# Kernel optimization log

Hardware: AMD Instinct MI355X
Metric: run time of the kernel (lower is better)

Reference implementation:

```python
import jax, jax.numpy as jnp
import numpy as np

HEADS = 8
DIM_K = 64
DIM_G = 64
INPLANES = 512
PLANES = 128  # int(inplanes * ratio)


def setup_inputs() -> dict:
    key = jax.random.key(0)
    ks = jax.random.split(key, 12)
    B, C, H, W = 16, INPLANES, 64, 64
    s = lambda fan: 1.0 / np.sqrt(fan)
    return {
        "x": jax.random.normal(ks[0], (B, C, H, W), dtype=jnp.float32),
        # conv_mask: Conv2d(C, HEADS, 1)
        "conv_mask_w": jax.random.normal(ks[1], (HEADS, C), dtype=jnp.float32) * s(C),
        "conv_mask_b": jnp.zeros((HEADS,), dtype=jnp.float32),
        # LinearG: dim_g -> 1
        "g_w": jax.random.normal(ks[2], (1, DIM_G), dtype=jnp.float32) * s(DIM_G),
        "g_b": jnp.zeros((1,), dtype=jnp.float32),
        # LinearK/Q/V: C -> dim_k
        "k_w": jax.random.normal(ks[3], (DIM_K, C), dtype=jnp.float32) * s(C),
        "k_b": jnp.zeros((DIM_K,), dtype=jnp.float32),
        "q_w": jax.random.normal(ks[4], (DIM_K, C), dtype=jnp.float32) * s(C),
        "q_b": jnp.zeros((DIM_K,), dtype=jnp.float32),
        "v_w": jax.random.normal(ks[5], (DIM_K, C), dtype=jnp.float32) * s(C),
        "v_b": jnp.zeros((DIM_K,), dtype=jnp.float32),
        # channel_add_conv: Conv2d(H*dk, planes, 1) -> LN([planes,1,1]) -> ReLU -> Conv2d(planes, C, 1)
        "add_w1": jax.random.normal(ks[6], (PLANES, HEADS * DIM_K), dtype=jnp.float32) * s(HEADS * DIM_K),
        "add_b1": jnp.zeros((PLANES,), dtype=jnp.float32),
        "ln_g": jnp.ones((PLANES,), dtype=jnp.float32),
        "ln_b": jnp.zeros((PLANES,), dtype=jnp.float32),
        "add_w2": jax.random.normal(ks[7], (C, PLANES), dtype=jnp.float32) * s(PLANES),
        "add_b2": jnp.zeros((C,), dtype=jnp.float32),
    }


def _forward(x, conv_mask_w, conv_mask_b, g_w, g_b, k_w, k_b, q_w, q_b,
             v_w, v_b, add_w1, add_b1, ln_g, ln_b, add_w2, add_b2):
    B, C, H, W = x.shape
    Hn, dk = HEADS, DIM_K
    # --- attention pooling mask ---
    logits = jnp.einsum('bchw,nc->bnhw', x, conv_mask_w) + conv_mask_b[None, :, None, None]
    mask = jax.nn.softmax(logits.reshape(B, Hn, H * W), axis=2)        # [B,Hn,HW]
    # per-head pooled context: [B,Hn,C]
    context = jnp.einsum('bcn,bhn->bhc', x.reshape(B, C, H * W), mask)
    # --- geometric position embedding ---
    mask4 = mask.reshape(B, Hn, H, W)
    cols = jnp.arange(W, dtype=x.dtype)   # mesh[...,0] = column index j
    rows = jnp.arange(H, dtype=x.dtype)   # mesh[...,1] = row index i
    cx = jnp.einsum('bnhw,w->bn', mask4, cols) / H
    cy = jnp.einsum('bnhw,h->bn', mask4, rows) / W
    dx = cx[:, :, None] - cx[:, None, :]
    dy = cy[:, :, None] - cy[:, None, :]
    # [B,Hn,Hn,4]
    pos = jnp.stack([jax.nn.relu(dx), jax.nn.relu(-dx),
                     jax.nn.relu(dy), jax.nn.relu(-dy)], axis=3)
    nfreq = DIM_G // 8
    dim_mat = 1.0 / (1000.0 ** (jnp.arange(nfreq, dtype=x.dtype) / nfreq))
    mul = (100.0 * pos[..., None]) * dim_mat                            # [B,Hn,Hn,4,nfreq]
    mul = mul.reshape(B, Hn, Hn, 4 * nfreq)
    emb = jnp.concatenate([jnp.sin(mul), jnp.cos(mul)], axis=-1)        # [B,Hn,Hn,DIM_G]
    w_g = jax.nn.relu(jnp.einsum('bmnd,od->bmno', emb, g_w)[..., 0] + g_b[0])  # [B,Hn,Hn]
    # --- head-level attention ---
    w_k = context @ k_w.T + k_b                                         # [B,Hn,dk]
    w_q = context @ q_w.T + q_b
    w_v = context @ v_w.T + v_b
    scaled_dot = jnp.einsum('bmd,bnd->bmn', w_k, w_q) / np.sqrt(dk)
    w_mn = jax.nn.softmax(jnp.log(jnp.clip(w_g, 1e-6)) + scaled_dot, axis=1)
    out_ctx = jnp.einsum('bmn,bmd->bnd', w_mn, w_v).reshape(B, Hn * dk)  # [B,512]
    # --- channel_add fusion (1x1 conv -> LN -> ReLU -> 1x1 conv), spatial dims are 1 ---
    y = out_ctx @ add_w1.T + add_b1                                     # [B,PLANES]
    mu = jnp.mean(y, axis=-1, keepdims=True)
    var = jnp.mean((y - mu) ** 2, axis=-1, keepdims=True)
    y = (y - mu) / jnp.sqrt(var + 1e-5) * ln_g + ln_b
    y = jax.nn.relu(y)
    add_term = y @ add_w2.T + add_b2                                    # [B,C]
    return x + add_term[:, :, None, None]


def reference(x, conv_mask_w, conv_mask_b, g_w, g_b, k_w, k_b, q_w, q_b,
              v_w, v_b, add_w1, add_b1, ln_g, ln_b, add_w2, add_b2):
    return _forward(x, conv_mask_w, conv_mask_b, g_w, g_b, k_w, k_b, q_w, q_b,
                    v_w, v_b, add_w1, add_b1, ln_g, ln_b, add_w2, add_b2)
```

## Files before the change

kernel.cpp:

```cpp
#include <hip/hip_runtime.h>
#include <cmath>

#define BB 16
#define CC 512
#define HWH 4096
#define NH 8
#define DK 64
#define PL 128

__device__ __forceinline__ float wred_sum(float v){
#pragma unroll
  for (int m = 32; m >= 1; m >>= 1) v += __shfl_xor(v, m, 64);
  return v;
}

__global__ __launch_bounds__(256) void k_logits(const float* __restrict__ x,
                                                const float* __restrict__ cmw,
                                                float* __restrict__ epart) {
  int bid = blockIdx.x;
  int cc = bid & 1;
  int tile = (bid >> 1) & 15;
  int b = bid >> 5;
  int p = tile * 256 + threadIdx.x;
  const float* xb = x + ((size_t)(b * CC + cc * 256)) * HWH + p;
  const float* wb = cmw + cc * 256;
  float acc[NH];
#pragma unroll
  for (int n = 0; n < NH; n++) acc[n] = 0.f;
#pragma unroll 8
  for (int c = 0; c < 256; c++) {
    float xv = xb[(size_t)c * HWH];
#pragma unroll
    for (int n = 0; n < NH; n++) acc[n] = fmaf(xv, wb[n * CC + c], acc[n]);
  }
  float* ob = epart + (((size_t)(cc * BB + b)) * NH) * HWH + p;
#pragma unroll
  for (int n = 0; n < NH; n++) ob[(size_t)n * HWH] = acc[n];
}

__global__ __launch_bounds__(256) void k_softmax(const float* __restrict__ epart,
                                                 float* __restrict__ e,
                                                 float* __restrict__ meta) {
  __shared__ float sr[4][4];
  int bn = blockIdx.x;
  int t = threadIdx.x;
  const float* r0 = epart + (size_t)bn * HWH;
  const float* r1 = r0 + (size_t)BB * NH * HWH;
  float* row = e + (size_t)bn * HWH;
  float v[16];
  float lmax = -1e30f;
#pragma unroll
  for (int i = 0; i < 16; i++) {
    int idx = t + 256 * i;
    v[i] = r0[idx] + r1[idx];
    lmax = fmaxf(lmax, v[i]);
  }
#pragma unroll
  for (int m = 32; m >= 1; m >>= 1) lmax = fmaxf(lmax, __shfl_xor(lmax, m, 64));
  if ((t & 63) == 0) sr[0][t >> 6] = lmax;
  __syncthreads();
  lmax = fmaxf(fmaxf(sr[0][0], sr[0][1]), fmaxf(sr[0][2], sr[0][3]));
  float s = 0.f, sc = 0.f, sy = 0.f;
#pragma unroll
  for (int i = 0; i < 16; i++) {
    int idx = t + 256 * i;
    float ev = expf(v[i] - lmax);
    row[idx] = ev;
    s += ev;
    sc += ev * (float)(idx & 63);
    sy += ev * (float)(idx >> 6);
  }
  s = wred_sum(s); sc = wred_sum(sc); sy = wred_sum(sy);
  if ((t & 63) == 0) { sr[1][t >> 6] = s; sr[2][t >> 6] = sc; sr[3][t >> 6] = sy; }
  __syncthreads();
  if (t == 0) {
    s  = sr[1][0] + sr[1][1] + sr[1][2] + sr[1][3];
    sc = sr[2][0] + sr[2][1] + sr[2][2] + sr[2][3];
    sy = sr[3][0] + sr[3][1] + sr[3][2] + sr[3][3];
    meta[bn]       = 1.f / s;
    meta[128 + bn] = sc / (s * 64.f);
    meta[256 + bn] = sy / (s * 64.f);
  }
}

__global__ __launch_bounds__(512) void k_context(const float* __restrict__ x,
                                                 const float* __restrict__ e,
                                                 float* __restrict__ pctx) {
  int bid = blockIdx.x;
  int ng = bid & 1;
  int cg = (bid >> 1) & 15;
  int b = bid >> 5;
  int w = threadIdx.x >> 6;
  int l = threadIdx.x & 63;
  int cbase = cg * 32 + w * 4;
  const float* xb = x + ((size_t)(b * CC + cbase)) * HWH + ng * 2048 + l * 4;
  const float* eb = e + (size_t)b * NH * HWH + ng * 2048 + l * 4;
  float acc[4][NH];
#pragma unroll
  for (int ci = 0; ci < 4; ci++)
#pragma unroll
    for (int h = 0; h < NH; h++) acc[ci][h] = 0.f;

#pragma unroll 2
  for (int ch = 0; ch < 8; ch++) {
    int off = ch * 256;
    float4 ev[NH];
#pragma unroll
    for (int h = 0; h < NH; h++)
      ev[h] = *reinterpret_cast<const float4*>(eb + (size_t)h * HWH + off);
#pragma unroll
    for (int ci = 0; ci < 4; ci++) {
      float4 xv = *reinterpret_cast<const float4*>(xb + (size_t)ci * HWH + off);
#pragma unroll
      for (int h = 0; h < NH; h++) {
        float a = acc[ci][h];
        a = fmaf(xv.x, ev[h].x, a);
        a = fmaf(xv.y, ev[h].y, a);
        a = fmaf(xv.z, ev[h].z, a);
        a = fmaf(xv.w, ev[h].w, a);
        acc[ci][h] = a;
      }
    }
  }
#pragma unroll
  for (int ci = 0; ci < 4; ci++)
#pragma unroll
    for (int h = 0; h < NH; h++) acc[ci][h] = wred_sum(acc[ci][h]);
  if (l == 0) {
    float* op = pctx + (((size_t)(ng * BB + b)) * NH) * CC + cbase;
#pragma unroll
    for (int h = 0; h < NH; h++)
#pragma unroll
      for (int ci = 0; ci < 4; ci++) op[h * CC + ci] = acc[ci][h];
  }
}

__global__ __launch_bounds__(512) void k_kqv(const float* __restrict__ pctx,
    const float* __restrict__ meta,
    const float* __restrict__ k_w, const float* __restrict__ q_w,
    const float* __restrict__ v_w,
    const float* __restrict__ k_b, const float* __restrict__ q_b,
    const float* __restrict__ v_b,
    float* __restrict__ kqvbuf) {
  int bid = blockIdx.x;
  int b = bid / 24;
  int r = bid - b * 24;
  int j = r >> 3;
  int h = r & 7;
  int t = threadIdx.x;
  __shared__ float ctx[8 * 68];
  __shared__ float psum[64][9];
  float inv = meta[b * NH + h];
  size_t base = ((size_t)b * NH + h) * CC + t;
  float cval = (pctx[base] + pctx[(size_t)BB * NH * CC + base]) * inv;
  ctx[(t >> 6) * 68 + (t & 63)] = cval;
  __syncthreads();
  const float* wm = (j == 0) ? k_w : (j == 1) ? q_w : v_w;
  const float* bm = (j == 0) ? k_b : (j == 1) ? q_b : v_b;
  int d = t >> 3, s = t & 7;
  const float* wr = wm + d * CC + s * 64;
  const float* cl = ctx + s * 68;
  float a = 0.f;
#pragma unroll
  for (int c = 0; c < 64; c += 4) {
    float4 w4 = *reinterpret_cast<const float4*>(wr + c);
    a = fmaf(w4.x, cl[c + 0], a);
    a = fmaf(w4.y, cl[c + 1], a);
    a = fmaf(w4.z, cl[c + 2], a);
    a = fmaf(w4.w, cl[c + 3], a);
  }
  psum[d][s] = a;
  __syncthreads();
  if (t < 64) {
    float rsum = 0.f;
#pragma unroll
    for (int ss = 0; ss < 8; ss++) rsum += psum[t][ss];
    kqvbuf[((size_t)(b * 3 + j) * NH + h) * DK + t] = rsum + bm[t];
  }
}

__global__ __launch_bounds__(512) void k_attn_mlp(const float* __restrict__ kqvbuf,
    const float* __restrict__ meta,
    const float* __restrict__ g_w, const float* __restrict__ g_b,
    const float* __restrict__ aw1, const float* __restrict__ ab1,
    const float* __restrict__ lng, const float* __restrict__ lnb,
    const float* __restrict__ aw2, const float* __restrict__ ab2,
    float* __restrict__ add_term) {
  int b = blockIdx.x;
  int t = threadIdx.x;
  __shared__ float kq[3][NH * 68];
  __shared__ float smn[NH][NH];
  __shared__ float cxl[NH], cyl[NH];
  __shared__ float oc[CC];
  __shared__ float part[4][PL];
  __shared__ float yl[PL];
  __shared__ float sr[2][2];

  if (t < NH) { cxl[t] = meta[128 + b * NH + t]; cyl[t] = meta[256 + b * NH + t]; }
  {
    int h = t >> 6, d = t & 63;
#pragma unroll
    for (int j = 0; j < 3; j++)
      kq[j][h * 68 + d] = kqvbuf[(size_t)(b * 3 + j) * 512 + t];
  }
  __syncthreads();

  if (t < 64) {
    int m = t >> 3, n = t & 7;
    float dx = cxl[m] - cxl[n];
    float dy = cyl[m] - cyl[n];
    float pos[4] = { fmaxf(dx, 0.f), fmaxf(-dx, 0.f), fmaxf(dy, 0.f), fmaxf(-dy, 0.f) };
    float a = g_b[0];
#pragma unroll
    for (int p = 0; p < 4; p++) {
#pragma unroll
      for (int f = 0; f < 8; f++) {
        float dm = expf(-0.8634694098727671f * (float)f);
        float ang = 100.f * pos[p] * dm;
        a = fmaf(sinf(ang), g_w[p * 8 + f], a);
        a = fmaf(cosf(ang), g_w[32 + p * 8 + f], a);
      }
    }
    float wgl = logf(fmaxf(fmaxf(a, 0.f), 1e-6f));
    float dot = 0.f;
#pragma unroll
    for (int dd = 0; dd < DK; dd++)
      dot = fmaf(kq[0][m * 68 + dd], kq[1][n * 68 + dd], dot);
    smn[m][n] = dot * 0.125f + wgl;
  }
  __syncthreads();
  if (t < 8) {
    float mx = -1e30f;
#pragma unroll
    for (int m = 0; m < NH; m++) mx = fmaxf(mx, smn[m][t]);
    float ssum = 0.f; float ex[NH];
#pragma unroll
    for (int m = 0; m < NH; m++) { ex[m] = expf(smn[m][t] - mx); ssum += ex[m]; }
#pragma unroll
    for (int m = 0; m < NH; m++) smn[m][t] = ex[m] / ssum;
  }
  __syncthreads();
  {
    int n = t >> 6, d = t & 63;
    float a = 0.f;
#pragma unroll
    for (int m = 0; m < NH; m++) a = fmaf(smn[m][n], kq[2][m * 68 + d], a);
    oc[t] = a;
  }
  __syncthreads();
  {
    int d = t & 127, p = t >> 7;
    const float* wr = aw1 + d * CC + p * 128;
    const float* ol = oc + p * 128;
    float a = 0.f;
#pragma unroll 8
    for (int c = 0; c < 128; c += 4) {
      float4 w4 = *reinterpret_cast<const float4*>(wr + c);
      a = fmaf(w4.x, ol[c + 0], a);
      a = fmaf(w4.y, ol[c + 1], a);
      a = fmaf(w4.z, ol[c + 2], a);
      a = fmaf(w4.w, ol[c + 3], a);
    }
    part[p][d] = a;
  }
  __syncthreads();
  float y = 0.f;
  if (t < PL) y = part[0][t] + part[1][t] + part[2][t] + part[3][t] + ab1[t];
  {
    float s  = (t < PL) ? y : 0.f;
    float sq = s * y;
    s = wred_sum(s); sq = wred_sum(sq);
    if (t < PL && (t & 63) == 0) { sr[0][t >> 6] = s; sr[1][t >> 6] = sq; }
  }
  __syncthreads();
  {
    float mu = (sr[0][0] + sr[0][1]) * (1.f / 128.f);
    float var = (sr[1][0] + sr[1][1]) * (1.f / 128.f) - mu * mu;
    float rstd = rsqrtf(var + 1e-5f);
    if (t < PL) yl[t] = fmaxf((y - mu) * rstd * lng[t] + lnb[t], 0.f);
  }
  __syncthreads();
  {
    const float* wr = aw2 + t * PL;
    float a = ab2[t];
#pragma unroll 8
    for (int pp = 0; pp < PL; pp += 4) {
      float4 w4 = *reinterpret_cast<const float4*>(wr + pp);
      a = fmaf(w4.x, yl[pp + 0], a);
      a = fmaf(w4.y, yl[pp + 1], a);
      a = fmaf(w4.z, yl[pp + 2], a);
      a = fmaf(w4.w, yl[pp + 3], a);
    }
    add_term[b * CC + t] = a;
  }
}

__global__ __launch_bounds__(256) void k_add(const float* __restrict__ x,
                                             const float* __restrict__ add_term,
                                             float* __restrict__ out) {
  const float4* x4 = reinterpret_cast<const float4*>(x);
  float4* o4 = reinterpret_cast<float4*>(out);
  const size_t n4 = (size_t)BB * CC * HWH / 4;
  for (size_t i = (size_t)blockIdx.x * 256 + threadIdx.x; i < n4;
       i += (size_t)gridDim.x * 256) {
    float4 v = x4[i];
    float a = add_term[i >> 10];
    v.x += a; v.y += a; v.z += a; v.w += a;
    o4[i] = v;
  }
}

extern "C" void kernel_launch(void* const* d_in, const int* in_sizes, int n_in,
                              void* d_out, int out_size, void* d_ws, size_t ws_size,
                              hipStream_t stream) {
  const float* x   = (const float*)d_in[0];
  const float* cmw = (const float*)d_in[1];
  const float* g_w = (const float*)d_in[3];
  const float* g_b = (const float*)d_in[4];
  const float* k_w = (const float*)d_in[5];
  const float* k_b = (const float*)d_in[6];
  const float* q_w = (const float*)d_in[7];
  const float* q_b = (const float*)d_in[8];
  const float* v_w = (const float*)d_in[9];
  const float* v_b = (const float*)d_in[10];
  const float* aw1 = (const float*)d_in[11];
  const float* ab1 = (const float*)d_in[12];
  const float* lng = (const float*)d_in[13];
  const float* lnb = (const float*)d_in[14];
  const float* aw2 = (const float*)d_in[15];
  const float* ab2 = (const float*)d_in[16];
  float* out = (float*)d_out;
  float* ws = (float*)d_ws;

  float* epart    = ws;
  float* e        = ws + 1048576;
  float* meta     = ws + 1572864;
  float* pctx     = ws;
  float* kqvbuf   = ws + 131072;
  float* add_term = ws + 155648;

  hipLaunchKernelGGL(k_logits,   dim3(512),  dim3(256), 0, stream, x, cmw, epart);
  hipLaunchKernelGGL(k_softmax,  dim3(128),  dim3(256), 0, stream, epart, e, meta);
  hipLaunchKernelGGL(k_context,  dim3(512),  dim3(512), 0, stream, x, e, pctx);
  hipLaunchKernelGGL(k_kqv,      dim3(384),  dim3(512), 0, stream, pctx, meta,
                     k_w, q_w, v_w, k_b, q_b, v_b, kqvbuf);
  hipLaunchKernelGGL(k_attn_mlp, dim3(16),   dim3(512), 0, stream, kqvbuf, meta,
                     g_w, g_b, aw1, ab1, lng, lnb, aw2, ab2, add_term);
  hipLaunchKernelGGL(k_add,      dim3(2048), dim3(256), 0, stream, x, add_term, out);
}
```

Before: 150.3 us.

## Vectorize logits kernel with float4, split channels 4-way, nontemporal output stores

The logits kernel now has each thread handle four pixels with float4 loads and stores, and splits channels into four 128-channel chunks, which halves the grid to 256 blocks. The softmax kernel sums four partial buffers instead of two using vector loads. The workspace offsets grow to hold the larger partial buffer. The final add kernel uses nontemporal stores so the large output write bypasses cache. The aim is to cut load instruction count and improve bandwidth use, at the cost of fewer blocks for occupancy and extra partial-sum traffic.

```diff
diff --git a/kernel.cpp b/kernel.cpp
--- a/kernel.cpp
+++ b/kernel.cpp
@@ -8,6 +8,8 @@
 #define DK 64
 #define PL 128
 
+typedef float fx4 __attribute__((ext_vector_type(4)));
+
 __device__ __forceinline__ float wred_sum(float v){
 #pragma unroll
   for (int m = 32; m >= 1; m >>= 1) v += __shfl_xor(v, m, 64);
@@ -18,24 +20,35 @@
                                                 const float* __restrict__ cmw,
                                                 float* __restrict__ epart) {
   int bid = blockIdx.x;
-  int cc = bid & 1;
-  int tile = (bid >> 1) & 15;
-  int b = bid >> 5;
-  int p = tile * 256 + threadIdx.x;
-  const float* xb = x + ((size_t)(b * CC + cc * 256)) * HWH + p;
-  const float* wb = cmw + cc * 256;
-  float acc[NH];
-#pragma unroll
-  for (int n = 0; n < NH; n++) acc[n] = 0.f;
-#pragma unroll 8
-  for (int c = 0; c < 256; c++) {
-    float xv = xb[(size_t)c * HWH];
-#pragma unroll
-    for (int n = 0; n < NH; n++) acc[n] = fmaf(xv, wb[n * CC + c], acc[n]);
+  int cc = bid & 3;
+  int tile = (bid >> 2) & 3;
+  int b = bid >> 4;
+  int p = tile * 1024 + threadIdx.x * 4;
+  const float* xb = x + ((size_t)(b * CC + cc * 128)) * HWH + p;
+  const float* wb = cmw + cc * 128;
+  float acc[NH][4];
+#pragma unroll
+  for (int n = 0; n < NH; n++)
+#pragma unroll
+    for (int k = 0; k < 4; k++) acc[n][k] = 0.f;
+#pragma unroll 4
+  for (int c = 0; c < 128; c++) {
+    float4 xv = *reinterpret_cast<const float4*>(xb + (size_t)c * HWH);
+#pragma unroll
+    for (int n = 0; n < NH; n++) {
+      float w = wb[n * CC + c];
+      acc[n][0] = fmaf(xv.x, w, acc[n][0]);
+      acc[n][1] = fmaf(xv.y, w, acc[n][1]);
+      acc[n][2] = fmaf(xv.z, w, acc[n][2]);
+      acc[n][3] = fmaf(xv.w, w, acc[n][3]);
+    }
   }
   float* ob = epart + (((size_t)(cc * BB + b)) * NH) * HWH + p;
 #pragma unroll
-  for (int n = 0; n < NH; n++) ob[(size_t)n * HWH] = acc[n];
+  for (int n = 0; n < NH; n++) {
+    float4 o = make_float4(acc[n][0], acc[n][1], acc[n][2], acc[n][3]);
+    *reinterpret_cast<float4*>(ob + (size_t)n * HWH) = o;
+  }
 }
 
 __global__ __launch_bounds__(256) void k_softmax(const float* __restrict__ epart,
@@ -44,16 +57,21 @@
   __shared__ float sr[4][4];
   int bn = blockIdx.x;
   int t = threadIdx.x;
-  const float* r0 = epart + (size_t)bn * HWH;
-  const float* r1 = r0 + (size_t)BB * NH * HWH;
   float* row = e + (size_t)bn * HWH;
-  float v[16];
+  float4 v[4];
   float lmax = -1e30f;
 #pragma unroll
-  for (int i = 0; i < 16; i++) {
-    int idx = t + 256 * i;
-    v[i] = r0[idx] + r1[idx];
-    lmax = fmaxf(lmax, v[i]);
+  for (int i = 0; i < 4; i++) {
+    int idx = t * 4 + i * 1024;
+    const float* r = epart + (size_t)bn * HWH + idx;
+    float4 a = *reinterpret_cast<const float4*>(r);
+#pragma unroll
+    for (int cc = 1; cc < 4; cc++) {
+      float4 pth = *reinterpret_cast<const float4*>(r + (size_t)cc * BB * NH * HWH);
+      a.x += pth.x; a.y += pth.y; a.z += pth.z; a.w += pth.w;
+    }
+    v[i] = a;
+    lmax = fmaxf(lmax, fmaxf(fmaxf(a.x, a.y), fmaxf(a.z, a.w)));
   }
 #pragma unroll
   for (int m = 32; m >= 1; m >>= 1) lmax = fmaxf(lmax, __shfl_xor(lmax, m, 64));
@@ -62,13 +80,19 @@
   lmax = fmaxf(fmaxf(sr[0][0], sr[0][1]), fmaxf(sr[0][2], sr[0][3]));
   float s = 0.f, sc = 0.f, sy = 0.f;
 #pragma unroll
-  for (int i = 0; i < 16; i++) {
-    int idx = t + 256 * i;
-    float ev = expf(v[i] - lmax);
-    row[idx] = ev;
-    s += ev;
-    sc += ev * (float)(idx & 63);
-    sy += ev * (float)(idx >> 6);
+  for (int i = 0; i < 4; i++) {
+    int idx = t * 4 + i * 1024;
+    float4 ev;
+    ev.x = expf(v[i].x - lmax);
+    ev.y = expf(v[i].y - lmax);
+    ev.z = expf(v[i].z - lmax);
+    ev.w = expf(v[i].w - lmax);
+    *reinterpret_cast<float4*>(row + idx) = ev;
+    float col = (float)(idx & 63);
+    float rw  = (float)(idx >> 6);
+    s += ev.x + ev.y + ev.z + ev.w;
+    sc += ev.x * col + ev.y * (col + 1.f) + ev.z * (col + 2.f) + ev.w * (col + 3.f);
+    sy += (ev.x + ev.y + ev.z + ev.w) * rw;
   }
   s = wred_sum(s); sc = wred_sum(sc); sy = wred_sum(sy);
   if ((t & 63) == 0) { sr[1][t >> 6] = s; sr[2][t >> 6] = sc; sr[3][t >> 6] = sy; }
@@ -298,15 +322,15 @@
 __global__ __launch_bounds__(256) void k_add(const float* __restrict__ x,
                                              const float* __restrict__ add_term,
                                              float* __restrict__ out) {
-  const float4* x4 = reinterpret_cast<const float4*>(x);
-  float4* o4 = reinterpret_cast<float4*>(out);
+  const fx4* x4 = reinterpret_cast<const fx4*>(x);
+  fx4* o4 = reinterpret_cast<fx4*>(out);
   const size_t n4 = (size_t)BB * CC * HWH / 4;
   for (size_t i = (size_t)blockIdx.x * 256 + threadIdx.x; i < n4;
        i += (size_t)gridDim.x * 256) {
-    float4 v = x4[i];
+    fx4 v = x4[i];
     float a = add_term[i >> 10];
-    v.x += a; v.y += a; v.z += a; v.w += a;
-    o4[i] = v;
+    v += a;
+    __builtin_nontemporal_store(v, &o4[i]);
   }
 }
 
@@ -333,13 +357,13 @@
   float* ws = (float*)d_ws;
 
   float* epart    = ws;
-  float* e        = ws + 1048576;
-  float* meta     = ws + 1572864;
+  float* e        = ws + 2097152;
+  float* meta     = ws + 2621440;
   float* pctx     = ws;
   float* kqvbuf   = ws + 131072;
   float* add_term = ws + 155648;
 
-  hipLaunchKernelGGL(k_logits,   dim3(512),  dim3(256), 0, stream, x, cmw, epart);
+  hipLaunchKernelGGL(k_logits,   dim3(256),  dim3(256), 0, stream, x, cmw, epart);
   hipLaunchKernelGGL(k_softmax,  dim3(128),  dim3(256), 0, stream, epart, e, meta);
   hipLaunchKernelGGL(k_context,  dim3(512),  dim3(512), 0, stream, x, e, pctx);
   hipLaunchKernelGGL(k_kqv,      dim3(384),  dim3(512), 0, stream, pctx, meta,
```

Result: slower. 163.1 us (+8.5%).
